# Kernel tuning notes

Measured on AMD Instinct MI355X. Metric: run time of the kernel, lower is better.

Reference implementation:

```python
import jax, jax.numpy as jnp
from jax import lax
import numpy as np
import math

IMG_H, IMG_W = 592, 800  # stride-16 image for a 50x37 feature map


def _make_anchors(fx=50, fy=37, base=8, dsr=16):
    rows = []
    for x in range(fx):
        for y in range(fy):
            for size in [base, 2 * base, 4 * base]:
                rows.append([(x - size / 2) * dsr, (y - size / 2) * dsr,
                             (x + size / 2) * dsr, (y + size / 2) * dsr])
                s = math.sqrt(size ** 2 / 2)
                rows.append([(x - s) * dsr, (y - s / 2) * dsr, (x + s) * dsr, (y + s / 2) * dsr])
                rows.append([(x - s / 2) * dsr, (y - s) * dsr, (x + s / 2) * dsr, (y + s) * dsr])
    return np.array(rows, np.float32)


def setup_inputs() -> dict:
    key = jax.random.key(0)
    k = jax.random.split(key, 8)
    B, G, H, W = 32, 20, 50, 37
    feats = jax.random.normal(k[0], (B, 512, H, W), jnp.float32)
    a = _make_anchors()
    keep = (a[:, 0] >= 0) & (a[:, 1] >= 0) & (a[:, 2] <= IMG_W) & (a[:, 3] <= IMG_H)
    idxs_inside = jnp.asarray(np.nonzero(keep)[0].astype(np.int32))
    anchors = jnp.asarray(a[keep])
    # valid xyxy GT boxes inside the image
    x1 = jax.random.uniform(k[1], (B, G)) * (IMG_W - 160)
    y1 = jax.random.uniform(k[2], (B, G)) * (IMG_H - 160)
    w = 32.0 + jax.random.uniform(k[3], (B, G)) * 96.0
    h = 32.0 + jax.random.uniform(k[4], (B, G)) * 96.0
    gt_boxes = jnp.stack([x1, y1, x1 + w, y1 + h], -1)
    W3 = jax.random.normal(k[5], (512, 512, 3, 3), jnp.float32) * 0.02
    b3 = jnp.zeros((512,), jnp.float32)
    Wcls = jax.random.normal(k[6], (18, 512, 1, 1), jnp.float32) * 0.02
    bcls = jnp.zeros((18,), jnp.float32)
    Wloc = jax.random.normal(k[7], (36, 512, 1, 1), jnp.float32) * 0.02
    bloc = jnp.zeros((36,), jnp.float32)
    return {"feats": feats, "gt_boxes": gt_boxes, "anchors": anchors,
            "W3": W3, "b3": b3, "Wcls": Wcls, "bcls": bcls,
            "Wloc": Wloc, "bloc": bloc, "idxs_inside": idxs_inside}


def _conv(x, w, b, pad):
    y = lax.conv_general_dilated(x, w, (1, 1), pad,
                                 dimension_numbers=("NCHW", "OIHW", "NCHW"))
    return y + b[None, :, None, None]


def reference(feats, gt_boxes, anchors, W3, b3, Wcls, bcls, Wloc, bloc, idxs_inside):
    B = feats.shape[0]
    rpn_conv1 = jax.nn.relu(_conv(feats, W3, b3, "SAME"))
    cls_score = _conv(rpn_conv1, Wcls, bcls, "VALID")          # [B,18,H,W]
    _, C, H, Wd = cls_score.shape
    logits = cls_score.reshape(B, 2, (C * H) // 2, Wd)          # reshape(x, 2)
    prob = jax.nn.softmax(logits, axis=1)
    prob_back = prob.reshape(B, C, H, Wd)                       # reshape back to 18
    loc_pred = _conv(rpn_conv1, Wloc, bloc, "VALID")            # [B,36,H,W]

    # select inside-image anchors
    logits_sel = logits.transpose(0, 2, 3, 1).reshape(B, -1, 2)[:, idxs_inside, :]
    loc_sel = loc_pred.transpose(0, 2, 3, 1).reshape(B, -1, 4)[:, idxs_inside, :]

    # vectorized anchors x gt IoU (replaces the triple python loop)
    ix1 = jnp.maximum(anchors[None, :, None, 0], gt_boxes[:, None, :, 0])
    iy1 = jnp.maximum(anchors[None, :, None, 1], gt_boxes[:, None, :, 1])
    ix2 = jnp.minimum(anchors[None, :, None, 2], gt_boxes[:, None, :, 2])
    iy2 = jnp.minimum(anchors[None, :, None, 3], gt_boxes[:, None, :, 3])
    inter = jnp.clip(ix2 - ix1, 0) * jnp.clip(iy2 - iy1, 0)     # [B,A,G]
    area_a = (anchors[:, 2] - anchors[:, 0]) * (anchors[:, 3] - anchors[:, 1])
    area_g = (gt_boxes[..., 2] - gt_boxes[..., 0]) * (gt_boxes[..., 3] - gt_boxes[..., 1])
    iou = inter / jnp.maximum(area_a[None, :, None] + area_g[:, None, :] - inter, 1e-8)

    max_iou = iou.max(-1)                                       # [B,A]
    matched = iou.argmax(-1)                                    # [B,A] gt index per anchor
    gt_best = iou.argmax(1)                                     # [B,G] best anchor per gt
    A = anchors.shape[0]
    is_best = jnp.zeros((B, A), bool).at[jnp.arange(B)[:, None], gt_best].set(True)
    labels = (is_best | (max_iou > 0.7)).astype(jnp.int32)      # positives=1, rest 0

    logsm = jax.nn.log_softmax(logits_sel, -1)
    loss_cls = -jnp.take_along_axis(logsm, labels[..., None], -1).mean()

    tgt = jnp.take_along_axis(gt_boxes, matched[:, :, None], axis=1)  # [B,A,4]
    d = loc_sel - tgt
    sl1 = jnp.where(jnp.abs(d) < 1.0, 0.5 * d * d, jnp.abs(d) - 0.5)
    loss_loc = (sl1 * labels[..., None].astype(sl1.dtype)).sum() / 256.0

    return prob_back, loc_pred, loss_cls, loss_loc
```

## Files before the change

### kernel.cpp

```cpp
#include <hip/hip_runtime.h>
#include <stdint.h>

typedef unsigned short u16;
typedef unsigned int   u32;
typedef unsigned long long u64;

typedef __bf16 v8bf __attribute__((ext_vector_type(8)));
typedef float  v4f  __attribute__((ext_vector_type(4)));

#define NBATCH 32
#define NCH    512
#define FH     50
#define FW     37
#define PIX    1850
#define MTOT   59200
#define KTOT   4608
#define HP     52
#define WP     39
#define NG     20
#define W3N    (NCH*KTOT)
#define WCBN   (64*512)
#define BORDN  364544
#define NT     72

#define PROB_N 1065600
#define LC_IDX 3196800
#define LL_IDX 3196801

__device__ __forceinline__ u16 f2bf(float f) {
    u32 u = __float_as_uint(f);
    u += 0x7fffu + ((u >> 16) & 1u);
    return (u16)(u >> 16);
}

__device__ __forceinline__ void gl_lds16(const u16* g, u16* l) {
    __builtin_amdgcn_global_load_lds((const __attribute__((address_space(1))) u32*)g,
                                     (__attribute__((address_space(3))) u32*)l,
                                     16, 0, 0);
}

__device__ __forceinline__ int offA_of(int T, int kh) {
    const int dydx = T >> 3;
    const int ci0  = (T & 7) << 6;
    return ((dydx / 3) * WP + (dydx % 3)) * NCH + ci0 + kh * 32;
}

__global__ __launch_bounds__(256) void pad_kernel(const float* __restrict__ feats,
                                                  u16* __restrict__ fpad) {
    __shared__ float t[64][65];
    const int b  = blockIdx.z;
    const int c0 = blockIdx.y * 64;
    const int p0 = blockIdx.x * 64;
    const int tid = threadIdx.x;
    {
        const int cl = tid >> 2, seg = tid & 3;
        const float* src = feats + ((size_t)b * NCH + c0 + cl) * PIX;
        const int pbase = p0 + seg * 16;
        #pragma unroll
        for (int i = 0; i < 16; i++) {
            int p = pbase + i;
            t[cl][seg * 16 + i] = (p < PIX) ? src[p] : 0.f;
        }
    }
    __syncthreads();
    {
        const int pl = tid >> 2, cs = tid & 3;
        const int p = p0 + pl;
        if (p < PIX) {
            const int h = p / FW, w = p % FW;
            size_t dst = (((size_t)b * HP + h + 1) * WP + (w + 1)) * NCH + c0 + cs * 16;
            u32 pk[8];
            #pragma unroll
            for (int i = 0; i < 8; i++) {
                u32 lo = f2bf(t[cs * 16 + 2 * i][pl]);
                u32 hi = f2bf(t[cs * 16 + 2 * i + 1][pl]);
                pk[i] = lo | (hi << 16);
            }
            *(uint4*)&fpad[dst]     = make_uint4(pk[0], pk[1], pk[2], pk[3]);
            *(uint4*)&fpad[dst + 8] = make_uint4(pk[4], pk[5], pk[6], pk[7]);
        }
    }
}

__global__ void prep_kernel(const float* __restrict__ w3, const float* __restrict__ wcls,
                            const float* __restrict__ wloc,
                            u16* __restrict__ wbt, u16* __restrict__ wcb,
                            u16* __restrict__ fpad, float* __restrict__ out) {
    int t = blockIdx.x * 256 + threadIdx.x;
    if (t < 2) out[LC_IDX + t] = 0.f;
    if (t < W3N) {
        int co = t / KTOT, k = t % KTOT;
        int dydx = k >> 9, ci = k & 511;
        wbt[t] = f2bf(w3[((size_t)co * NCH + ci) * 9 + dydx]);
    } else if (t < W3N + WCBN) {
        int t2 = t - W3N;
        int c = t2 >> 9, ci = t2 & 511;
        float v = (c < 18) ? wcls[c * 512 + ci]
                : (c < 54) ? wloc[(c - 18) * 512 + ci] : 0.f;
        wcb[t2] = f2bf(v);
    } else if (t < W3N + WCBN + BORDN) {
        int t3 = t - (W3N + WCBN);
        int c8 = t3 & 63;
        int pi = (t3 >> 6) % 178;
        int b  = (t3 >> 6) / 178;
        int h, w;
        if (pi < 39)       { h = 0;        w = pi; }
        else if (pi < 78)  { h = 51;       w = pi - 39; }
        else if (pi < 128) { h = pi - 77;  w = 0; }
        else               { h = pi - 127; w = 38; }
        size_t dst = (((size_t)b * HP + h) * WP + w) * NCH + c8 * 8;
        *(uint4*)&fpad[dst] = make_uint4(0, 0, 0, 0);
    }
}

__global__ __launch_bounds__(512, 2) void conv3x3_mfma(const u16* __restrict__ fpad,
                                                       const u16* __restrict__ wbt,
                                                       const float* __restrict__ b3,
                                                       u16* __restrict__ conv1) {
    __shared__ __align__(16) u16 As[2][2][256][32];
    __shared__ __align__(16) u16 Bs[2][2][256][32];

    const int wg     = ((int)blockIdx.x & 7) * 58 + ((int)blockIdx.x >> 3);
    const int n_base = (wg & 1) * 256;
    const int m_base = (wg >> 1) * 256;

    const int tid = threadIdx.x;
    const int w   = tid >> 6;
    const int l   = tid & 63;

    const int sr   = l >> 2;
    const int sseg = (l & 3) ^ ((l >> 3) & 3);
    int rbA[2], rbB[2];
    #pragma unroll
    for (int c = 0; c < 2; c++) {
        const int r  = w * 32 + c * 16 + sr;
        const int m  = m_base + r;
        const int mm = (m < MTOT) ? m : 0;
        const int b = mm / PIX, p = mm % PIX;
        const int y = p / FW, x = p % FW;
        rbA[c] = ((b * HP + y) * WP + x) * NCH + sseg * 8;
        rbB[c] = (n_base + r) * KTOT + sseg * 8;
    }
    u16* const aBase = &As[0][0][0][0] + w * 1024;
    u16* const bBase = &Bs[0][0][0][0] + w * 1024;

    const int wm = w >> 2, wn = w & 3;
    const int lm = l & 15, quad = l >> 4;
    const int psw = (quad ^ ((lm >> 1) & 3)) * 8;
    const u16* const aR = &As[0][0][0][0] + (wm * 128 + lm) * 32 + psw;
    const u16* const bR = &Bs[0][0][0][0] + (wn * 64  + lm) * 32 + psw;

    v4f acc[8][4];
    #pragma unroll
    for (int i = 0; i < 8; i++)
        #pragma unroll
        for (int j = 0; j < 4; j++)
            #pragma unroll
            for (int r = 0; r < 4; r++) acc[i][j][r] = 0.f;

#define STAGE_A(buf, kh, Tp) { \
        const int oA_ = offA_of((Tp), (kh)); \
        u16* const dA_ = aBase + (buf) * 16384 + (kh) * 8192; \
        gl_lds16(fpad + rbA[0] + oA_, dA_); \
        gl_lds16(fpad + rbA[1] + oA_, dA_ + 512); }
#define STAGE_B(buf, kh, Tp) { \
        const int oB_ = (Tp) * 64 + (kh) * 32; \
        u16* const dB_ = bBase + (buf) * 16384 + (kh) * 8192; \
        gl_lds16(wbt + rbB[0] + oB_, dB_); \
        gl_lds16(wbt + rbB[1] + oB_, dB_ + 512); }
#define RD_A(dst, buf, kh, mh) { \
        _Pragma("unroll") \
        for (int i_ = 0; i_ < 4; i_++) \
            dst[i_] = *(const v8bf*)(aR + (buf) * 16384 + (kh) * 8192 + ((mh) * 4 + i_) * 512); }
#define RD_B(dst, buf, kh) { \
        _Pragma("unroll") \
        for (int j_ = 0; j_ < 4; j_++) \
            dst[j_] = *(const v8bf*)(bR + (buf) * 16384 + (kh) * 8192 + j_ * 512); }
#define MM(afv, bfv, mh) { \
        _Pragma("unroll") \
        for (int i_ = 0; i_ < 4; i_++) \
            _Pragma("unroll") \
            for (int j_ = 0; j_ < 4; j_++) \
                acc[(mh) * 4 + i_][j_] = __builtin_amdgcn_mfma_f32_16x16x32_bf16( \
                    afv[i_], bfv[j_], acc[(mh) * 4 + i_][j_], 0, 0, 0); }

    STAGE_A(0, 0, 0); STAGE_B(0, 0, 0);
    STAGE_A(0, 1, 0); STAGE_B(0, 1, 0);

    for (int T = 0; T < NT; ++T) {
        const int cb = T & 1;
        const int nb = cb ^ 1;
        asm volatile("s_waitcnt vmcnt(0)" ::: "memory");
        __builtin_amdgcn_s_barrier();
        if (T + 1 < NT) {
            STAGE_A(nb, 0, T + 1); STAGE_B(nb, 0, T + 1);
            STAGE_A(nb, 1, T + 1); STAGE_B(nb, 1, T + 1);
        }
        v8bf b0[4], b1[4], a00[4], a01[4], a10[4], a11[4];
        RD_B(b0, cb, 0); RD_A(a00, cb, 0, 0); RD_A(a01, cb, 0, 1);
        RD_B(b1, cb, 1); RD_A(a10, cb, 1, 0); RD_A(a11, cb, 1, 1);
        MM(a00, b0, 0);
        MM(a01, b0, 1);
        MM(a10, b1, 0);
        MM(a11, b1, 1);
    }
#undef MM
#undef RD_B
#undef RD_A
#undef STAGE_B
#undef STAGE_A

    #pragma unroll
    for (int nj = 0; nj < 4; nj++) {
        const int n = n_base + wn * 64 + nj * 16 + lm;
        const float bias = b3[n];
        #pragma unroll
        for (int i = 0; i < 8; i++) {
            #pragma unroll
            for (int r = 0; r < 4; r++) {
                const int m = m_base + wm * 128 + i * 16 + quad * 4 + r;
                if (m < MTOT) {
                    float v = acc[i][nj][r] + bias;
                    v = v > 0.f ? v : 0.f;
                    conv1[(size_t)m * NCH + n] = f2bf(v);
                }
            }
        }
    }
}

__global__ __launch_bounds__(256) void head_mfma(const u16* __restrict__ conv1,
                                                 const u16* __restrict__ wcb,
                                                 const float* __restrict__ bcls,
                                                 const float* __restrict__ bloc,
                                                 float* __restrict__ out) {
    __shared__ __align__(16) u16 As[128][64];
    __shared__ __align__(16) u16 Bs[64][64];
    __shared__ float ct[128][66];

    const int tid = threadIdx.x;
    const int m_base = blockIdx.x * 128;
    const int wave = tid >> 6;
    const int lane = tid & 63;
    const int srow  = tid >> 3;
    const int seg_g = (tid & 7) ^ (srow & 7);

    int rbA[4];
    #pragma unroll
    for (int r = 0; r < 4; r++) {
        int m = m_base + r * 32 + srow;
        int mm = (m < MTOT) ? m : 0;
        rbA[r] = mm * NCH + seg_g * 8;
    }
    int rbB[2];
    #pragma unroll
    for (int r = 0; r < 2; r++)
        rbB[r] = (r * 32 + srow) * NCH + seg_g * 8;

    u16* const asb = &As[0][0] + wave * 512;
    u16* const bsb = &Bs[0][0] + wave * 512;

    const int wn = wave * 16;
    const int lm = lane & 15;
    const int quad = lane >> 4;
    const int x7 = lm & 7;

    v4f acc[8];
    #pragma unroll
    for (int i = 0; i < 8; i++)
        #pragma unroll
        for (int r = 0; r < 4; r++) acc[i][r] = 0.f;

    for (int k0 = 0; k0 < NCH; k0 += 64) {
        #pragma unroll
        for (int r = 0; r < 4; r++)
            gl_lds16(conv1 + rbA[r] + k0, asb + r * 2048);
        #pragma unroll
        for (int r = 0; r < 2; r++)
            gl_lds16(wcb + rbB[r] + k0, bsb + r * 2048);
        __syncthreads();

        #pragma unroll
        for (int kh = 0; kh < 2; kh++) {
            const int ps = (((kh << 2) | quad) ^ x7) * 8;
            v8bf bf = *(const v8bf*)(&Bs[0][0] + (wn + lm) * 64 + ps);
            #pragma unroll
            for (int i = 0; i < 8; i++) {
                v8bf af = *(const v8bf*)(&As[0][0] + (i * 16 + lm) * 64 + ps);
                acc[i] = __builtin_amdgcn_mfma_f32_16x16x32_bf16(af, bf, acc[i], 0, 0, 0);
            }
        }
        __syncthreads();
    }

    const int col = wn + lm;
    const float bias = (col < 18) ? bcls[col] : (col < 54) ? bloc[col - 18] : 0.f;
    #pragma unroll
    for (int i = 0; i < 8; i++)
        #pragma unroll
        for (int r = 0; r < 4; r++)
            ct[i * 16 + quad * 4 + r][col] = acc[i][r] + bias;
    __syncthreads();

    const int c = tid >> 2;
    const int pix4 = tid & 3;
    for (int px = pix4; px < 128; px += 4) {
        const int m = m_base + px;
        if (m >= MTOT) break;
        const int b = m / PIX;
        const int p = m - b * PIX;
        if (c < 9) {
            float s0 = ct[px][c], s1 = ct[px][c + 9];
            float mx = fmaxf(s0, s1);
            float e0 = __expf(s0 - mx), e1 = __expf(s1 - mx);
            float inv = 1.f / (e0 + e1);
            out[((size_t)b * 18 + c) * PIX + p]     = e0 * inv;
            out[((size_t)b * 18 + c + 9) * PIX + p] = e1 * inv;
        } else if (c >= 18 && c < 54) {
            out[(size_t)PROB_N + ((size_t)b * 36 + (c - 18)) * PIX + p] = ct[px][c];
        }
    }
}

__global__ __launch_bounds__(256) void iouloss_kernel(const float* __restrict__ anchors,
                                                      const float* __restrict__ gtb,
                                                      const int* __restrict__ idxs,
                                                      int A,
                                                      const float* __restrict__ outr,
                                                      float* __restrict__ out) {
    __shared__ float g[NG * 4];
    __shared__ u64 keys[NG];
    __shared__ int gbest[NG];
    __shared__ float red[8];
    const int b = blockIdx.y;
    const int tid = threadIdx.x;
    if (tid < NG * 4) g[tid] = gtb[b * NG * 4 + tid];
    if (tid < NG) keys[tid] = 0ull;
    __syncthreads();

    u64 lk[NG];
    #pragma unroll
    for (int gi = 0; gi < NG; gi++) lk[gi] = 0ull;
    for (int a = tid; a < A; a += 256) {
        const float ax1 = anchors[a * 4 + 0], ay1 = anchors[a * 4 + 1];
        const float ax2 = anchors[a * 4 + 2], ay2 = anchors[a * 4 + 3];
        const float areaA = (ax2 - ax1) * (ay2 - ay1);
        const u64 atag = (u64)(0xFFFFFFFFu - (u32)a);
        #pragma unroll
        for (int gi = 0; gi < NG; gi++) {
            float gx1 = g[gi*4], gy1 = g[gi*4+1], gx2 = g[gi*4+2], gy2 = g[gi*4+3];
            float iw = fmaxf(fminf(ax2, gx2) - fmaxf(ax1, gx1), 0.f);
            float ih = fmaxf(fminf(ay2, gy2) - fmaxf(ay1, gy1), 0.f);
            float inter = iw * ih;
            float areaG = (gx2 - gx1) * (gy2 - gy1);
            float iou = inter / fmaxf(areaA + areaG - inter, 1e-8f);
            u64 key = (((u64)__float_as_uint(iou)) << 32) | atag;
            if (key > lk[gi]) lk[gi] = key;
        }
    }
    #pragma unroll
    for (int gi = 0; gi < NG; gi++) {
        u64 k = lk[gi];
        #pragma unroll
        for (int off = 32; off; off >>= 1) {
            u64 o = __shfl_xor(k, off);
            k = (o > k) ? o : k;
        }
        if ((tid & 63) == 0) atomicMax(&keys[gi], k);
    }
    __syncthreads();
    if (tid < NG) gbest[tid] = (int)(0xFFFFFFFFu - (u32)(keys[tid] & 0xFFFFFFFFull));
    __syncthreads();

    float lc = 0.f, ll = 0.f;
    for (int a = tid; a < A; a += 256) {
        const float ax1 = anchors[a * 4 + 0], ay1 = anchors[a * 4 + 1];
        const float ax2 = anchors[a * 4 + 2], ay2 = anchors[a * 4 + 3];
        const float areaA = (ax2 - ax1) * (ay2 - ay1);
        float best = -1.f;
        int bg = 0;
        #pragma unroll
        for (int gi = 0; gi < NG; gi++) {
            float gx1 = g[gi*4], gy1 = g[gi*4+1], gx2 = g[gi*4+2], gy2 = g[gi*4+3];
            float iw = fmaxf(fminf(ax2, gx2) - fmaxf(ax1, gx1), 0.f);
            float ih = fmaxf(fminf(ay2, gy2) - fmaxf(ay1, gy1), 0.f);
            float inter = iw * ih;
            float areaG = (gx2 - gx1) * (gy2 - gy1);
            float iou = inter / fmaxf(areaA + areaG - inter, 1e-8f);
            if (iou > best) { best = iou; bg = gi; }
        }
        int lbl = (best > 0.7f) ? 1 : 0;
        if (!lbl) {
            #pragma unroll
            for (int gi = 0; gi < NG; gi++) lbl |= (gbest[gi] == a);
        }
        const int idx = idxs[a];
        const int cpr = idx / PIX;
        const int rem = idx % PIX;
        float p0 = outr[((size_t)b * 18 + cpr) * PIX + rem];
        float p1 = outr[((size_t)b * 18 + cpr + 9) * PIX + rem];
        lc += -logf(lbl ? p1 : p0);
        if (lbl) {
            const int hh = idx / 333;
            const int r2 = idx % 333;
            const int ww = r2 / 9;
            const int c4 = r2 % 9;
            const int pp = hh * FW + ww;
            #pragma unroll
            for (int t = 0; t < 4; t++) {
                float lv = outr[(size_t)PROB_N + ((size_t)b * 36 + c4 * 4 + t) * PIX + pp];
                float d = lv - g[bg * 4 + t];
                float ad = fabsf(d);
                ll += (ad < 1.f) ? 0.5f * d * d : ad - 0.5f;
            }
        }
    }
    #pragma unroll
    for (int off = 32; off; off >>= 1) {
        lc += __shfl_xor(lc, off);
        ll += __shfl_xor(ll, off);
    }
    const int lane = tid & 63, wave = tid >> 6;
    if (lane == 0) { red[wave] = lc; red[4 + wave] = ll; }
    __syncthreads();
    if (tid == 0) {
        float slc = red[0] + red[1] + red[2] + red[3];
        float sll = red[4] + red[5] + red[6] + red[7];
        atomicAdd(&out[LC_IDX], slc * (1.f / (32.f * (float)A)));
        atomicAdd(&out[LL_IDX], sll * (1.f / 256.f));
    }
}

extern "C" void kernel_launch(void* const* d_in, const int* in_sizes, int n_in,
                              void* d_out, int out_size, void* d_ws, size_t ws_size,
                              hipStream_t stream) {
    const float* feats   = (const float*)d_in[0];
    const float* gtb     = (const float*)d_in[1];
    const float* anchors = (const float*)d_in[2];
    const float* W3      = (const float*)d_in[3];
    const float* b3      = (const float*)d_in[4];
    const float* Wcls    = (const float*)d_in[5];
    const float* bcls    = (const float*)d_in[6];
    const float* Wloc    = (const float*)d_in[7];
    const float* bloc    = (const float*)d_in[8];
    const int*   idxs    = (const int*)d_in[9];
    const int A = in_sizes[9];
    float* out = (float*)d_out;

    char* ws = (char*)d_ws;
    size_t off = 0;
    auto alloc = [&](size_t bytes) -> void* {
        void* p = ws + off;
        off = (off + bytes + 255) & ~(size_t)255;
        return p;
    };
    const size_t fpad_n = (size_t)NBATCH * HP * WP * NCH;
    u16* fpad   = (u16*)alloc(fpad_n * 2);
    u16* wbt    = (u16*)alloc((size_t)W3N * 2);
    u16* wcb    = (u16*)alloc((size_t)WCBN * 2);
    u16* conv1  = (u16*)alloc((size_t)MTOT * NCH * 2);

    const int prep_tot = W3N + WCBN + BORDN;
    prep_kernel<<<(prep_tot + 255) / 256, 256, 0, stream>>>(W3, Wcls, Wloc, wbt, wcb, fpad, out);
    pad_kernel<<<dim3(29, 8, NBATCH), 256, 0, stream>>>(feats, fpad);
    conv3x3_mfma<<<464, 512, 0, stream>>>(fpad, wbt, b3, conv1);
    head_mfma<<<463, 256, 0, stream>>>(conv1, wcb, bcls, bloc, out);
    iouloss_kernel<<<dim3(1, NBATCH), 256, 0, stream>>>(anchors, gtb, idxs, A, out, out);
}
```

Baseline: 819.1 us.

## Store conv tiles as 64-wide K rows and pre-tile weights per K-step

The shared-memory tiles change from two 32-element K halves to single 64-element rows, using a new XOR swizzle for bank-conflict avoidance. Each staging load row now covers 128 contiguous bytes of the padded activations. The 3x3 weights are re-laid out in the prep kernel as [K-step][out-channel][64], so each K-step's B tile is one contiguous 64KB block. The aim is better global coalescing and fewer LDS conflicts, but the new swizzle and index math carry correctness risk.

```diff
diff --git a/kernel.cpp b/kernel.cpp
--- a/kernel.cpp
+++ b/kernel.cpp
@@ -39,10 +39,14 @@
                                      16, 0, 0);
 }
 
-__device__ __forceinline__ int offA_of(int T, int kh) {
+__device__ __forceinline__ int offA_of(int T) {
     const int dydx = T >> 3;
     const int ci0  = (T & 7) << 6;
-    return ((dydx / 3) * WP + (dydx % 3)) * NCH + ci0 + kh * 32;
+    return ((dydx / 3) * WP + (dydx % 3)) * NCH + ci0;
+}
+
+__device__ __forceinline__ int Srow(int r) {
+    return ((r >> 1) & 3) | ((r & 1) << 2);
 }
 
 __global__ __launch_bounds__(256) void pad_kernel(const float* __restrict__ feats,
@@ -89,9 +93,12 @@
     int t = blockIdx.x * 256 + threadIdx.x;
     if (t < 2) out[LC_IDX + t] = 0.f;
     if (t < W3N) {
-        int co = t / KTOT, k = t % KTOT;
+        int T = t >> 15;
+        int n = (t >> 6) & 511;
+        int c = t & 63;
+        int k = T * 64 + c;
         int dydx = k >> 9, ci = k & 511;
-        wbt[t] = f2bf(w3[((size_t)co * NCH + ci) * 9 + dydx]);
+        wbt[t] = f2bf(w3[((size_t)n * NCH + ci) * 9 + dydx]);
     } else if (t < W3N + WCBN) {
         int t2 = t - W3N;
         int c = t2 >> 9, ci = t2 & 511;
@@ -117,8 +124,8 @@
                                                        const u16* __restrict__ wbt,
                                                        const float* __restrict__ b3,
                                                        u16* __restrict__ conv1) {
-    __shared__ __align__(16) u16 As[2][2][256][32];
-    __shared__ __align__(16) u16 Bs[2][2][256][32];
+    __shared__ __align__(16) u16 As[2][256][64];
+    __shared__ __align__(16) u16 Bs[2][256][64];
 
     const int wg     = ((int)blockIdx.x & 7) * 58 + ((int)blockIdx.x >> 3);
     const int n_base = (wg & 1) * 256;
@@ -128,27 +135,29 @@
     const int w   = tid >> 6;
     const int l   = tid & 63;
 
-    const int sr   = l >> 2;
-    const int sseg = (l & 3) ^ ((l >> 3) & 3);
-    int rbA[2], rbB[2];
-    #pragma unroll
-    for (int c = 0; c < 2; c++) {
-        const int r  = w * 32 + c * 16 + sr;
-        const int m  = m_base + r;
+    int rbA[4], rbB[4];
+    #pragma unroll
+    for (int c = 0; c < 4; c++) {
+        const int row = w * 32 + c * 8 + (l >> 3);
+        const int g   = (l & 7) ^ Srow(row);
+        const int m  = m_base + row;
         const int mm = (m < MTOT) ? m : 0;
         const int b = mm / PIX, p = mm % PIX;
         const int y = p / FW, x = p % FW;
-        rbA[c] = ((b * HP + y) * WP + x) * NCH + sseg * 8;
-        rbB[c] = (n_base + r) * KTOT + sseg * 8;
-    }
-    u16* const aBase = &As[0][0][0][0] + w * 1024;
-    u16* const bBase = &Bs[0][0][0][0] + w * 1024;
+        rbA[c] = ((b * HP + y) * WP + x) * NCH + g * 8;
+        rbB[c] = (n_base + row) * 64 + g * 8;
+    }
+    u16* const aBase = &As[0][0][0] + w * 2048;
+    u16* const bBase = &Bs[0][0][0] + w * 2048;
 
     const int wm = w >> 2, wn = w & 3;
     const int lm = l & 15, quad = l >> 4;
-    const int psw = (quad ^ ((lm >> 1) & 3)) * 8;
-    const u16* const aR = &As[0][0][0][0] + (wm * 128 + lm) * 32 + psw;
-    const u16* const bR = &Bs[0][0][0][0] + (wn * 64  + lm) * 32 + psw;
+    const int Sl = Srow(lm & 7);
+    int ps[2];
+    ps[0] = (quad ^ Sl) * 8;
+    ps[1] = ((4 + quad) ^ Sl) * 8;
+    const u16* const aR = &As[0][0][0] + (wm * 128 + lm) * 64;
+    const u16* const bR = &Bs[0][0][0] + (wn * 64  + lm) * 64;
 
     v4f acc[8][4];
     #pragma unroll
@@ -158,24 +167,28 @@
             #pragma unroll
             for (int r = 0; r < 4; r++) acc[i][j][r] = 0.f;
 
-#define STAGE_A(buf, kh, Tp) { \
-        const int oA_ = offA_of((Tp), (kh)); \
-        u16* const dA_ = aBase + (buf) * 16384 + (kh) * 8192; \
+#define STAGE_A(buf, Tp) { \
+        const int oA_ = offA_of(Tp); \
+        u16* const dA_ = aBase + (buf) * 16384; \
         gl_lds16(fpad + rbA[0] + oA_, dA_); \
-        gl_lds16(fpad + rbA[1] + oA_, dA_ + 512); }
-#define STAGE_B(buf, kh, Tp) { \
-        const int oB_ = (Tp) * 64 + (kh) * 32; \
-        u16* const dB_ = bBase + (buf) * 16384 + (kh) * 8192; \
-        gl_lds16(wbt + rbB[0] + oB_, dB_); \
-        gl_lds16(wbt + rbB[1] + oB_, dB_ + 512); }
+        gl_lds16(fpad + rbA[1] + oA_, dA_ + 512); \
+        gl_lds16(fpad + rbA[2] + oA_, dA_ + 1024); \
+        gl_lds16(fpad + rbA[3] + oA_, dA_ + 1536); }
+#define STAGE_B(buf, Tp) { \
+        const u16* const sB_ = wbt + (size_t)(Tp) * 32768; \
+        u16* const dB_ = bBase + (buf) * 16384; \
+        gl_lds16(sB_ + rbB[0], dB_); \
+        gl_lds16(sB_ + rbB[1], dB_ + 512); \
+        gl_lds16(sB_ + rbB[2], dB_ + 1024); \
+        gl_lds16(sB_ + rbB[3], dB_ + 1536); }
 #define RD_A(dst, buf, kh, mh) { \
         _Pragma("unroll") \
         for (int i_ = 0; i_ < 4; i_++) \
-            dst[i_] = *(const v8bf*)(aR + (buf) * 16384 + (kh) * 8192 + ((mh) * 4 + i_) * 512); }
+            dst[i_] = *(const v8bf*)(aR + (buf) * 16384 + ((mh) * 4 + i_) * 1024 + ps[kh]); }
 #define RD_B(dst, buf, kh) { \
         _Pragma("unroll") \
         for (int j_ = 0; j_ < 4; j_++) \
-            dst[j_] = *(const v8bf*)(bR + (buf) * 16384 + (kh) * 8192 + j_ * 512); }
+            dst[j_] = *(const v8bf*)(bR + (buf) * 16384 + j_ * 1024 + ps[kh]); }
 #define MM(afv, bfv, mh) { \
         _Pragma("unroll") \
         for (int i_ = 0; i_ < 4; i_++) \
@@ -184,8 +197,7 @@
                 acc[(mh) * 4 + i_][j_] = __builtin_amdgcn_mfma_f32_16x16x32_bf16( \
                     afv[i_], bfv[j_], acc[(mh) * 4 + i_][j_], 0, 0, 0); }
 
-    STAGE_A(0, 0, 0); STAGE_B(0, 0, 0);
-    STAGE_A(0, 1, 0); STAGE_B(0, 1, 0);
+    STAGE_A(0, 0); STAGE_B(0, 0);
 
     for (int T = 0; T < NT; ++T) {
         const int cb = T & 1;
@@ -193,8 +205,7 @@
         asm volatile("s_waitcnt vmcnt(0)" ::: "memory");
         __builtin_amdgcn_s_barrier();
         if (T + 1 < NT) {
-            STAGE_A(nb, 0, T + 1); STAGE_B(nb, 0, T + 1);
-            STAGE_A(nb, 1, T + 1); STAGE_B(nb, 1, T + 1);
+            STAGE_A(nb, T + 1); STAGE_B(nb, T + 1);
         }
         v8bf b0[4], b1[4], a00[4], a01[4], a10[4], a11[4];
         RD_B(b0, cb, 0); RD_A(a00, cb, 0, 0); RD_A(a01, cb, 0, 1);
```

New measurement: 760.3 us. 7.2% less time.
